# Optimization experiments

Measured on AMD Instinct MI355X. Metric: run time of the kernel, lower is better.

The kernel has to match this reference:

```python
import jax, jax.numpy as jnp
import numpy as np

EPS = 1e-10


def setup_inputs() -> dict:
    key = jax.random.key(0)
    k1, k2 = jax.random.split(key)
    S, B, D = 512, 4096, 64
    support_set = jax.random.normal(k1, (S, B, D), dtype=jnp.float32)
    X_hat = jax.random.normal(k2, (B, D), dtype=jnp.float32)
    return {"support_set": support_set, "X_hat": X_hat, "normalize": 1}


def reference(support_set, X_hat, normalize):
    # Batched cosine similarity replacing the per-step Python loop.
    # support_set: [S, B, D], X_hat: [B, D] -> similarities: [S, B]
    dot = jnp.einsum('sbd,bd->sb', support_set, X_hat)
    support_norm = jnp.sqrt(jnp.sum(support_set * support_set, axis=-1))  # [S, B]
    x_norm = jnp.sqrt(jnp.sum(X_hat * X_hat, axis=-1))                    # [B]
    # F.cosine_similarity clamps each norm to eps before dividing.
    denom = jnp.maximum(support_norm, EPS) * jnp.maximum(x_norm, EPS)[None, :]
    sim = dot / denom
    if normalize:
        sim = (sim + 1.0) * 0.5
    return sim
```

## Files before the change

kernel.cpp:

```cpp
#include <hip/hip_runtime.h>


#define EPS_F 1e-10f

static constexpr int kB = 4096;
static constexpr int kD = 64;
static constexpr int kS = 512;

__global__ __launch_bounds__(256) void cosine_sim_kernel(
    const float* __restrict__ support,
    const float* __restrict__ xhat,
    const int* __restrict__ normalize_p,
    float* __restrict__ out,
    int total_rows)
{
    const int norm_flag = *normalize_p;
    const int tid       = blockIdx.x * blockDim.x + threadIdx.x;
    const int lane_q    = threadIdx.x & 15;
    const int row0      = tid >> 4;
    const int row_step  = (gridDim.x * blockDim.x) >> 4;

    for (int row = row0; row < total_rows; row += row_step) {
        const int b = row & (kB - 1);

        const float4 sv = *reinterpret_cast<const float4*>(
            support + (size_t)row * kD + (size_t)lane_q * 4);
        const float4 xv = *reinterpret_cast<const float4*>(
            xhat + (size_t)b * kD + (size_t)lane_q * 4);

        float dot = sv.x * xv.x + sv.y * xv.y + sv.z * xv.z + sv.w * xv.w;
        float sn  = sv.x * sv.x + sv.y * sv.y + sv.z * sv.z + sv.w * sv.w;
        float xn  = xv.x * xv.x + xv.y * xv.y + xv.z * xv.z + xv.w * xv.w;

        #pragma unroll
        for (int m = 1; m < 16; m <<= 1) {
            dot += __shfl_xor(dot, m, 64);
            sn  += __shfl_xor(sn,  m, 64);
            xn  += __shfl_xor(xn,  m, 64);
        }

        if (lane_q == 0) {
            const float denom = fmaxf(sqrtf(sn), EPS_F) * fmaxf(sqrtf(xn), EPS_F);
            float sim = dot / denom;
            if (norm_flag) sim = (sim + 1.0f) * 0.5f;
            out[row] = sim;
        }
    }
}

extern "C" void kernel_launch(void* const* d_in, const int* in_sizes, int n_in,
                              void* d_out, int out_size, void* d_ws, size_t ws_size,
                              hipStream_t stream) {
    const float* support  = (const float*)d_in[0];
    const float* xhat     = (const float*)d_in[1];
    const int*   norm_ptr = (const int*)d_in[2];
    float*       out      = (float*)d_out;

    const int total_rows = kS * kB;

    const int block = 256;
    const int grid  = 2048;
    cosine_sim_kernel<<<grid, block, 0, stream>>>(support, xhat, norm_ptr, out,
                                                  total_rows);
}
```

Measured before the change: 681.5 us.

## Remap threads to b-tiles over s-chunks and hoist X_hat norm

Each block now owns 16 batch rows and loops over a chunk of 64 support slices, so X_hat is loaded and its norm reduced once per thread instead of per row. The inner loop drops one shuffle reduction and uses a precomputed reciprocal. The loop is unrolled to keep more loads in flight, but the grid shape changes, which may affect memory parallelism.

```diff
diff --git a/kernel.cpp b/kernel.cpp
--- a/kernel.cpp
+++ b/kernel.cpp
@@ -6,44 +6,51 @@
 static constexpr int kB = 4096;
 static constexpr int kD = 64;
 static constexpr int kS = 512;
+static constexpr int S_CHUNKS = 8;
+static constexpr int S_PER    = kS / S_CHUNKS;
+static constexpr int B_TILES  = kB / 16;
 
 __global__ __launch_bounds__(256) void cosine_sim_kernel(
     const float* __restrict__ support,
     const float* __restrict__ xhat,
     const int* __restrict__ normalize_p,
-    float* __restrict__ out,
-    int total_rows)
+    float* __restrict__ out)
 {
+    const int t      = threadIdx.x;
+    const int lq     = t & 15;
+    const int g      = t >> 4;
+    const int b_tile = blockIdx.x & (B_TILES - 1);
+    const int s0     = (blockIdx.x >> 8) * S_PER;
+    const int b      = b_tile * 16 + g;
+
+    const float4 xv = *reinterpret_cast<const float4*>(xhat + b * kD + lq * 4);
+    float xn = xv.x * xv.x + xv.y * xv.y + xv.z * xv.z + xv.w * xv.w;
+    #pragma unroll
+    for (int m = 1; m < 16; m <<= 1) xn += __shfl_xor(xn, m, 64);
+    const float xinv = 1.0f / fmaxf(sqrtf(xn), EPS_F);
+
     const int norm_flag = *normalize_p;
-    const int tid       = blockIdx.x * blockDim.x + threadIdx.x;
-    const int lane_q    = threadIdx.x & 15;
-    const int row0      = tid >> 4;
-    const int row_step  = (gridDim.x * blockDim.x) >> 4;
 
-    for (int row = row0; row < total_rows; row += row_step) {
-        const int b = row & (kB - 1);
+    const float* sp = support + ((size_t)s0 * kB + b) * kD + (size_t)lq * 4;
+    float*       op = out + (size_t)s0 * kB + b;
 
-        const float4 sv = *reinterpret_cast<const float4*>(
-            support + (size_t)row * kD + (size_t)lane_q * 4);
-        const float4 xv = *reinterpret_cast<const float4*>(
-            xhat + (size_t)b * kD + (size_t)lane_q * 4);
+    #pragma unroll 4
+    for (int i = 0; i < S_PER; ++i) {
+        const float4 sv = *reinterpret_cast<const float4*>(sp + (size_t)i * (kB * kD));
 
         float dot = sv.x * xv.x + sv.y * xv.y + sv.z * xv.z + sv.w * xv.w;
         float sn  = sv.x * sv.x + sv.y * sv.y + sv.z * sv.z + sv.w * sv.w;
-        float xn  = xv.x * xv.x + xv.y * xv.y + xv.z * xv.z + xv.w * xv.w;
 
         #pragma unroll
         for (int m = 1; m < 16; m <<= 1) {
             dot += __shfl_xor(dot, m, 64);
             sn  += __shfl_xor(sn,  m, 64);
-            xn  += __shfl_xor(xn,  m, 64);
         }
 
-        if (lane_q == 0) {
-            const float denom = fmaxf(sqrtf(sn), EPS_F) * fmaxf(sqrtf(xn), EPS_F);
-            float sim = dot / denom;
-            if (norm_flag) sim = (sim + 1.0f) * 0.5f;
-            out[row] = sim;
+        if (lq == 0) {
+            float sim = dot * xinv / fmaxf(sqrtf(sn), EPS_F);
+            if (norm_flag) sim = fmaf(sim, 0.5f, 0.5f);
+            op[(size_t)i * kB] = sim;
         }
     }
 }
@@ -56,10 +63,7 @@
     const int*   norm_ptr = (const int*)d_in[2];
     float*       out      = (float*)d_out;
 
-    const int total_rows = kS * kB;
-
     const int block = 256;
-    const int grid  = 2048;
-    cosine_sim_kernel<<<grid, block, 0, stream>>>(support, xhat, norm_ptr, out,
-                                                  total_rows);
+    const int grid  = B_TILES * S_CHUNKS;
+    cosine_sim_kernel<<<grid, block, 0, stream>>>(support, xhat, norm_ptr, out);
 }
```

Result: no change. 692.4 us (+1.6%).
